# Kernel optimization log

Measured on AMD Instinct MI355X. Metric: run time of the kernel, lower is better.

The kernel has to match this reference:

```python
import jax, jax.numpy as jnp
import numpy as np


def setup_inputs() -> dict:
    key = jax.random.key(0)
    k1, k2 = jax.random.split(key)
    B, T, D, E = 4, 4096, 2048, 64
    x = jax.random.normal(k1, (B, T, D), dtype=jnp.float32)
    # nn.Linear default init ~ U(-1/sqrt(D), 1/sqrt(D)); scaled normal is fine for a numeric baseline
    W = jax.random.normal(k2, (D, E), dtype=jnp.float32) * (1.0 / np.sqrt(D))
    b = jnp.zeros((E,), dtype=jnp.float32)
    return {"x": x, "W": W, "b": b}


TOPK = 2


def reference(x, W, b):
    # logits: (B, T, E)
    logits = jnp.einsum("btd,de->bte", x, W) + b
    probs = jax.nn.softmax(logits, axis=-1)
    topk_vals, topk_idx = jax.lax.top_k(probs, TOPK)
    return topk_idx, topk_vals
```

## Files before the change

kernel.cpp:

```cpp
#include <hip/hip_runtime.h>
#include <math.h>


#define D_DIM 2048
#define E_DIM 64
#define M_DIM 16384
#define RM 32
#define BKC 64
#define NCHW 8
#define XSTR 68

typedef _Float16 half8 __attribute__((ext_vector_type(8)));
typedef float floatx4 __attribute__((ext_vector_type(4)));
typedef unsigned int uint;

__global__ __launch_bounds__(256) void split_w_kernel(
    const float* __restrict__ Wm, _Float16* __restrict__ wsT)
{
    const int tid = threadIdx.x;
    const int n   = tid & 63;
    const int kk0 = tid >> 6;
    const int g   = blockIdx.x;
    #pragma unroll
    for (int r = 0; r < 8; r++) {
        const int kk = kk0 + r * 4;
        const float v = Wm[(size_t)(g * 32 + kk) * E_DIM + n];
        const _Float16 h = (_Float16)v;
        const _Float16 l = (_Float16)((v - (float)h) * 2048.0f);
        const int t = n >> 4, cc = n & 15, qd = kk >> 3, j = kk & 7;
        const size_t base = (size_t)((g * 4 + t) * 2) * 512 + (size_t)(qd * 16 + cc) * 8 + j;
        wsT[base]       = h;
        wsT[base + 512] = l;
    }
}

__global__ __launch_bounds__(256, 2) void router_mfma_kernel(
    const float* __restrict__ x, const _Float16* __restrict__ wsT,
    const float* __restrict__ bias, float* __restrict__ out)
{
    __shared__ uint xbuf[4][2][RM * XSTR];

    const int lane = threadIdx.x & 63;
    const int wave = threadIdx.x >> 6;
    const int c    = lane & 15;
    const int quad = lane >> 4;
    const int r0   = blockIdx.x * RM;
    const int kb   = wave * (D_DIM / 4);

    const float* xg = x + (size_t)(r0 + quad) * D_DIM + kb + c * 4;
    const _Float16* wbase = wsT + (size_t)(wave * 16) * 4096 + lane * 8;

    floatx4 accm[2][4] = {};
    floatx4 accl[2][4] = {};
    float4 xa[8], xb[8];
    half8 wh0[4], wl0[4], wh1[4], wl1[4];

    auto loadx = [&](int n, float4* dst) {
        const int nn = n < NCHW ? n : NCHW - 1;
        #pragma unroll
        for (int i = 0; i < 8; i++)
            dst[i] = *reinterpret_cast<const float4*>(xg + (size_t)i * 4 * D_DIM + nn * BKC);
    };
    auto stage = [&](int buf, const float4* src) {
        uint* dst = &xbuf[wave][buf][0];
        #pragma unroll
        for (int i = 0; i < 8; i++) {
            const int row = i * 4 + quad;
            const float v[4] = {src[i].x, src[i].y, src[i].z, src[i].w};
            uint p[4];
            #pragma unroll
            for (int q = 0; q < 4; q++) {
                const _Float16 h = (_Float16)v[q];
                const _Float16 l = (_Float16)((v[q] - (float)h) * 2048.0f);
                p[q] = (uint)__builtin_bit_cast(unsigned short, h)
                     | ((uint)__builtin_bit_cast(unsigned short, l) << 16);
            }
            *reinterpret_cast<uint4*>(dst + row * XSTR + c * 4) =
                make_uint4(p[0], p[1], p[2], p[3]);
        }
    };
    auto loadW = [&](int u, half8* wh, half8* wl) {
        const int uu = u < 16 ? u : 15;
        const _Float16* p = wbase + (size_t)uu * 4096;
        #pragma unroll
        for (int t = 0; t < 4; t++) {
            wh[t] = *reinterpret_cast<const half8*>(p + t * 1024);
            wl[t] = *reinterpret_cast<const half8*>(p + t * 1024 + 512);
        }
    };
    auto step = [&](int buf, int s, const half8* wh, const half8* wl) {
        #pragma unroll
        for (int tau = 0; tau < 2; tau++) {
            const uint* rp = &xbuf[wave][buf][(tau * 16 + c) * XSTR + s * 32 + quad * 8];
            uint u8[8];
            *reinterpret_cast<uint4*>(u8)     = *reinterpret_cast<const uint4*>(rp);
            *reinterpret_cast<uint4*>(u8 + 4) = *reinterpret_cast<const uint4*>(rp + 4);
            uint hh[4], ll[4];
            #pragma unroll
            for (int q = 0; q < 4; q++) {
                hh[q] = (u8[2 * q] & 0xffffu) | (u8[2 * q + 1] << 16);
                ll[q] = (u8[2 * q] >> 16) | (u8[2 * q + 1] & 0xffff0000u);
            }
            const half8 ah = __builtin_bit_cast(half8, make_uint4(hh[0], hh[1], hh[2], hh[3]));
            const half8 al = __builtin_bit_cast(half8, make_uint4(ll[0], ll[1], ll[2], ll[3]));
            #pragma unroll
            for (int t = 0; t < 4; t++) {
                accm[tau][t] = __builtin_amdgcn_mfma_f32_16x16x32_f16(ah, wh[t], accm[tau][t], 0, 0, 0);
                accl[tau][t] = __builtin_amdgcn_mfma_f32_16x16x32_f16(al, wh[t], accl[tau][t], 0, 0, 0);
                accl[tau][t] = __builtin_amdgcn_mfma_f32_16x16x32_f16(ah, wl[t], accl[tau][t], 0, 0, 0);
            }
        }
    };

    loadx(0, xa);
    loadx(1, xb);
    loadW(0, wh0, wl0);
    stage(0, xa);

    #pragma unroll 1
    for (int n = 0; n < NCHW; n += 2) {
        loadx(n + 2, xa);
        loadW(2 * n + 1, wh1, wl1);
        stage(1, xb);
        step(0, 0, wh0, wl0);
        loadW(2 * n + 2, wh0, wl0);
        step(0, 1, wh1, wl1);
        loadx(n + 3, xb);
        loadW(2 * n + 3, wh1, wl1);
        if (n + 2 < NCHW) stage(0, xa);
        step(1, 0, wh0, wl0);
        loadW(2 * n + 4, wh0, wl0);
        step(1, 1, wh1, wl1);
    }

    __syncthreads();
    float* red = reinterpret_cast<float*>(&xbuf[0][0][0]);
    const float scale = 1.0f / 2048.0f;
    #pragma unroll
    for (int tau = 0; tau < 2; tau++)
        #pragma unroll
        for (int t = 0; t < 4; t++)
            #pragma unroll
            for (int i = 0; i < 4; i++)
                red[(wave * 32 + tau * 16 + quad * 4 + i) * 65 + c + 16 * t] =
                    accm[tau][t][i] + accl[tau][t][i] * scale;
    __syncthreads();

    if (wave >= 2) return;

    float bvt[4];
    #pragma unroll
    for (int t = 0; t < 4; t++) bvt[t] = bias[c + 16 * t];

    #pragma unroll
    for (int i = 0; i < 4; i++) {
        const int row = wave * 16 + quad * 4 + i;
        float lt[4];
        #pragma unroll
        for (int t = 0; t < 4; t++) {
            const int col = c + 16 * t;
            lt[t] = red[(0 * 32 + row) * 65 + col] + red[(1 * 32 + row) * 65 + col]
                  + red[(2 * 32 + row) * 65 + col] + red[(3 * 32 + row) * 65 + col] + bvt[t];
        }
        const float l0 = lt[0], l1 = lt[1], l2 = lt[2], l3 = lt[3];

        float m = fmaxf(fmaxf(l0, l1), fmaxf(l2, l3));
        #pragma unroll
        for (int off = 1; off < 16; off <<= 1)
            m = fmaxf(m, __shfl_xor(m, off, 64));

        const float e0 = expf(l0 - m), e1 = expf(l1 - m);
        const float e2 = expf(l2 - m), e3 = expf(l3 - m);
        float s = e0 + e1 + e2 + e3;
        #pragma unroll
        for (int off = 1; off < 16; off <<= 1)
            s += __shfl_xor(s, off, 64);

        const float p0 = e0 / s, p1 = e1 / s, p2 = e2 / s, p3 = e3 / s;

        const unsigned long long ka =
            ((unsigned long long)__float_as_uint(p0) << 32) | (unsigned long long)(63 - c);
        const unsigned long long kb_ =
            ((unsigned long long)__float_as_uint(p1) << 32) | (unsigned long long)(47 - c);
        const unsigned long long kc_ =
            ((unsigned long long)__float_as_uint(p2) << 32) | (unsigned long long)(31 - c);
        const unsigned long long kd =
            ((unsigned long long)__float_as_uint(p3) << 32) | (unsigned long long)(15 - c);

        unsigned long long hi1 = ka > kb_ ? ka : kb_, lo1 = ka > kb_ ? kb_ : ka;
        unsigned long long hi2 = kc_ > kd ? kc_ : kd, lo2 = kc_ > kd ? kd : kc_;
        unsigned long long k1 = hi1 > hi2 ? hi1 : hi2;
        unsigned long long mn = hi1 > hi2 ? hi2 : hi1;
        unsigned long long mx = lo1 > lo2 ? lo1 : lo2;
        unsigned long long k2 = mn > mx ? mn : mx;

        #pragma unroll
        for (int off = 1; off < 16; off <<= 1) {
            const unsigned long long o1 = __shfl_xor(k1, off, 64);
            const unsigned long long o2 = __shfl_xor(k2, off, 64);
            const unsigned long long n1 = k1 > o1 ? k1 : o1;
            const unsigned long long w1 = k1 > o1 ? o1 : k1;
            const unsigned long long w2 = k2 > o2 ? k2 : o2;
            k1 = n1;
            k2 = w1 > w2 ? w1 : w2;
        }

        if (c == 0) {
            const int gr = r0 + row;
            out[gr * 2 + 0] = (float)(63 - (int)(k1 & 0xFFFFFFFFull));
            out[gr * 2 + 1] = (float)(63 - (int)(k2 & 0xFFFFFFFFull));
            out[M_DIM * 2 + gr * 2 + 0] = __uint_as_float((unsigned)(k1 >> 32));
            out[M_DIM * 2 + gr * 2 + 1] = __uint_as_float((unsigned)(k2 >> 32));
        }
    }
}

extern "C" void kernel_launch(void* const* d_in, const int* in_sizes, int n_in,
                              void* d_out, int out_size, void* d_ws, size_t ws_size,
                              hipStream_t stream) {
    const float* x  = (const float*)d_in[0];
    const float* Wm = (const float*)d_in[1];
    const float* b  = (const float*)d_in[2];
    float* out = (float*)d_out;
    _Float16* wsT = (_Float16*)d_ws;

    split_w_kernel<<<dim3(64), dim3(256), 0, stream>>>(Wm, wsT);
    router_mfma_kernel<<<dim3(M_DIM / RM), dim3(256), 0, stream>>>(x, wsT, b, out);
}
```

Measured before the change: 202.7 us.

## Halve rows per block to 16 and restructure chunk pipeline for higher occupancy

Cuts each block's row tile from 32 to 16 and its per-chunk K width from 64 to 32, which doubles the chunk count to 16 and removes the second 16-row accumulator set. The loop now does one MFMA step per chunk, the staging and LDS layout shrink to match, and launch bounds ask for 3 blocks per SIMD instead of 2. The goal is fewer registers and more resident waves to hide global-load latency. In exchange each W fragment loaded is reused across half as many rows, so L2 traffic for W per output row doubles, and the grid doubles.

```diff
diff --git a/kernel.cpp b/kernel.cpp
--- a/kernel.cpp
+++ b/kernel.cpp
@@ -5,10 +5,10 @@
 #define D_DIM 2048
 #define E_DIM 64
 #define M_DIM 16384
-#define RM 32
-#define BKC 64
-#define NCHW 8
-#define XSTR 68
+#define RM 16
+#define BKC 32
+#define NCH 16
+#define XSTR 34
 
 typedef _Float16 half8 __attribute__((ext_vector_type(8)));
 typedef float floatx4 __attribute__((ext_vector_type(4)));
@@ -34,7 +34,7 @@
     }
 }
 
-__global__ __launch_bounds__(256, 2) void router_mfma_kernel(
+__global__ __launch_bounds__(256, 3) void router_mfma_kernel(
     const float* __restrict__ x, const _Float16* __restrict__ wsT,
     const float* __restrict__ bias, float* __restrict__ out)
 {
@@ -47,25 +47,25 @@
     const int r0   = blockIdx.x * RM;
     const int kb   = wave * (D_DIM / 4);
 
-    const float* xg = x + (size_t)(r0 + quad) * D_DIM + kb + c * 4;
+    const float* xg = x + (size_t)(r0 + (lane >> 3)) * D_DIM + kb + (lane & 7) * 4;
     const _Float16* wbase = wsT + (size_t)(wave * 16) * 4096 + lane * 8;
 
-    floatx4 accm[2][4] = {};
-    floatx4 accl[2][4] = {};
-    float4 xa[8], xb[8];
+    floatx4 accm[4] = {};
+    floatx4 accl[4] = {};
+    float4 xa[2], xb[2];
     half8 wh0[4], wl0[4], wh1[4], wl1[4];
 
     auto loadx = [&](int n, float4* dst) {
-        const int nn = n < NCHW ? n : NCHW - 1;
-        #pragma unroll
-        for (int i = 0; i < 8; i++)
-            dst[i] = *reinterpret_cast<const float4*>(xg + (size_t)i * 4 * D_DIM + nn * BKC);
+        const int nn = n < NCH ? n : NCH - 1;
+        #pragma unroll
+        for (int i = 0; i < 2; i++)
+            dst[i] = *reinterpret_cast<const float4*>(xg + (size_t)i * 8 * D_DIM + nn * BKC);
     };
     auto stage = [&](int buf, const float4* src) {
         uint* dst = &xbuf[wave][buf][0];
         #pragma unroll
-        for (int i = 0; i < 8; i++) {
-            const int row = i * 4 + quad;
+        for (int i = 0; i < 2; i++) {
+            const int row = i * 8 + (lane >> 3);
             const float v[4] = {src[i].x, src[i].y, src[i].z, src[i].w};
             uint p[4];
             #pragma unroll
@@ -75,12 +75,12 @@
                 p[q] = (uint)__builtin_bit_cast(unsigned short, h)
                      | ((uint)__builtin_bit_cast(unsigned short, l) << 16);
             }
-            *reinterpret_cast<uint4*>(dst + row * XSTR + c * 4) =
+            *reinterpret_cast<uint4*>(dst + row * XSTR + (lane & 7) * 4) =
                 make_uint4(p[0], p[1], p[2], p[3]);
         }
     };
     auto loadW = [&](int u, half8* wh, half8* wl) {
-        const int uu = u < 16 ? u : 15;
+        const int uu = u < NCH ? u : NCH - 1;
         const _Float16* p = wbase + (size_t)uu * 4096;
         #pragma unroll
         for (int t = 0; t < 4; t++) {
@@ -88,27 +88,24 @@
             wl[t] = *reinterpret_cast<const half8*>(p + t * 1024 + 512);
         }
     };
-    auto step = [&](int buf, int s, const half8* wh, const half8* wl) {
-        #pragma unroll
-        for (int tau = 0; tau < 2; tau++) {
-            const uint* rp = &xbuf[wave][buf][(tau * 16 + c) * XSTR + s * 32 + quad * 8];
-            uint u8[8];
-            *reinterpret_cast<uint4*>(u8)     = *reinterpret_cast<const uint4*>(rp);
-            *reinterpret_cast<uint4*>(u8 + 4) = *reinterpret_cast<const uint4*>(rp + 4);
-            uint hh[4], ll[4];
-            #pragma unroll
-            for (int q = 0; q < 4; q++) {
-                hh[q] = (u8[2 * q] & 0xffffu) | (u8[2 * q + 1] << 16);
-                ll[q] = (u8[2 * q] >> 16) | (u8[2 * q + 1] & 0xffff0000u);
-            }
-            const half8 ah = __builtin_bit_cast(half8, make_uint4(hh[0], hh[1], hh[2], hh[3]));
-            const half8 al = __builtin_bit_cast(half8, make_uint4(ll[0], ll[1], ll[2], ll[3]));
-            #pragma unroll
-            for (int t = 0; t < 4; t++) {
-                accm[tau][t] = __builtin_amdgcn_mfma_f32_16x16x32_f16(ah, wh[t], accm[tau][t], 0, 0, 0);
-                accl[tau][t] = __builtin_amdgcn_mfma_f32_16x16x32_f16(al, wh[t], accl[tau][t], 0, 0, 0);
-                accl[tau][t] = __builtin_amdgcn_mfma_f32_16x16x32_f16(ah, wl[t], accl[tau][t], 0, 0, 0);
-            }
+    auto step = [&](int buf, const half8* wh, const half8* wl) {
+        const uint* rp = &xbuf[wave][buf][c * XSTR + quad * 8];
+        uint u8[8];
+        *reinterpret_cast<uint4*>(u8)     = *reinterpret_cast<const uint4*>(rp);
+        *reinterpret_cast<uint4*>(u8 + 4) = *reinterpret_cast<const uint4*>(rp + 4);
+        uint hh[4], ll[4];
+        #pragma unroll
+        for (int q = 0; q < 4; q++) {
+            hh[q] = (u8[2 * q] & 0xffffu) | (u8[2 * q + 1] << 16);
+            ll[q] = (u8[2 * q] >> 16) | (u8[2 * q + 1] & 0xffff0000u);
+        }
+        const half8 ah = __builtin_bit_cast(half8, make_uint4(hh[0], hh[1], hh[2], hh[3]));
+        const half8 al = __builtin_bit_cast(half8, make_uint4(ll[0], ll[1], ll[2], ll[3]));
+        #pragma unroll
+        for (int t = 0; t < 4; t++) {
+            accm[t] = __builtin_amdgcn_mfma_f32_16x16x32_f16(ah, wh[t], accm[t], 0, 0, 0);
+            accl[t] = __builtin_amdgcn_mfma_f32_16x16x32_f16(al, wh[t], accl[t], 0, 0, 0);
+            accl[t] = __builtin_amdgcn_mfma_f32_16x16x32_f16(ah, wl[t], accl[t], 0, 0, 0);
         }
     };
 
@@ -118,35 +115,29 @@
     stage(0, xa);
 
     #pragma unroll 1
-    for (int n = 0; n < NCHW; n += 2) {
+    for (int n = 0; n < NCH; n += 2) {
         loadx(n + 2, xa);
-        loadW(2 * n + 1, wh1, wl1);
+        loadW(n + 1, wh1, wl1);
         stage(1, xb);
-        step(0, 0, wh0, wl0);
-        loadW(2 * n + 2, wh0, wl0);
-        step(0, 1, wh1, wl1);
+        step(0, wh0, wl0);
         loadx(n + 3, xb);
-        loadW(2 * n + 3, wh1, wl1);
-        if (n + 2 < NCHW) stage(0, xa);
-        step(1, 0, wh0, wl0);
-        loadW(2 * n + 4, wh0, wl0);
-        step(1, 1, wh1, wl1);
+        loadW(n + 2, wh0, wl0);
+        if (n + 2 < NCH) stage(0, xa);
+        step(1, wh1, wl1);
     }
 
     __syncthreads();
     float* red = reinterpret_cast<float*>(&xbuf[0][0][0]);
     const float scale = 1.0f / 2048.0f;
     #pragma unroll
-    for (int tau = 0; tau < 2; tau++)
-        #pragma unroll
-        for (int t = 0; t < 4; t++)
-            #pragma unroll
-            for (int i = 0; i < 4; i++)
-                red[(wave * 32 + tau * 16 + quad * 4 + i) * 65 + c + 16 * t] =
-                    accm[tau][t][i] + accl[tau][t][i] * scale;
+    for (int t = 0; t < 4; t++)
+        #pragma unroll
+        for (int i = 0; i < 4; i++)
+            red[(wave * 16 + quad * 4 + i) * 65 + c + 16 * t] =
+                accm[t][i] + accl[t][i] * scale;
     __syncthreads();
 
-    if (wave >= 2) return;
+    if (wave != 0) return;
 
     float bvt[4];
     #pragma unroll
@@ -154,13 +145,13 @@
 
     #pragma unroll
     for (int i = 0; i < 4; i++) {
-        const int row = wave * 16 + quad * 4 + i;
+        const int row = quad * 4 + i;
         float lt[4];
         #pragma unroll
         for (int t = 0; t < 4; t++) {
             const int col = c + 16 * t;
-            lt[t] = red[(0 * 32 + row) * 65 + col] + red[(1 * 32 + row) * 65 + col]
-                  + red[(2 * 32 + row) * 65 + col] + red[(3 * 32 + row) * 65 + col] + bvt[t];
+            lt[t] = red[(0 * 16 + row) * 65 + col] + red[(1 * 16 + row) * 65 + col]
+                  + red[(2 * 16 + row) * 65 + col] + red[(3 * 16 + row) * 65 + col] + bvt[t];
         }
         const float l0 = lt[0], l1 = lt[1], l2 = lt[2], l3 = lt[3];
 
```

Measured after the change: 211.5 us. +4.4%, slower.
